# Kernel tuning notes

Hardware: AMD Instinct MI355X
Metric: run time of the kernel (lower is better)

The kernel has to match this reference:

```python
import jax, jax.numpy as jnp
import numpy as np

N, D, K, NUM_CB = 65536, 256, 1024, 3

def setup_inputs() -> dict:
    key = jax.random.key(0)
    k1, k2 = jax.random.split(key)
    z = jax.random.normal(k1, (N, D), dtype=jnp.float32)
    # torch init: uniform_(-1/codebook_size, 1/codebook_size)
    codebooks = jax.random.uniform(k2, (NUM_CB, K, D), dtype=jnp.float32,
                                   minval=-1.0 / K, maxval=1.0 / K)
    return {"z": z, "codebooks": codebooks}

def reference(z, codebooks):
    """Residual VQ quantize() of RVQ_VAE: 3 sequential codebook stages with
    straight-through estimator. Returns (final_quantized, codebook_loss, commitment_loss)."""
    sg = jax.lax.stop_gradient
    final_quantized = jnp.zeros_like(z)
    codebook_losses = jnp.asarray(0.0, z.dtype)
    commitment_losses = jnp.asarray(0.0, z.dtype)
    for i in range(codebooks.shape[0]):  # small fixed number of residual stages
        cb = codebooks[i]                               # [K, D]
        # squared L2 distances via the matmul expansion (as in the torch code)
        l2 = jnp.sum(z * z, axis=1, keepdims=True)      # [N, 1]
        c2 = jnp.sum(cb * cb, axis=1)[None, :]          # [1, K]
        cl = z @ cb.T                                   # [N, K] GEMM
        distances = l2 - 2.0 * cl + c2                  # [N, K]
        closest = jnp.argmin(distances, axis=-1)        # [N]
        # one-hot @ codebook in the original == direct gather (same math)
        codes = cb[closest]                             # [N, D]
        codebook_losses = codebook_losses + jnp.mean((codes - sg(z)) ** 2)
        commitment_losses = commitment_losses + jnp.mean((sg(codes) - z) ** 2)
        codes_st = z + sg(codes - z)                    # straight-through
        final_quantized = final_quantized + codes_st
        z = z - sg(codes_st)                            # residual for next stage
    return final_quantized, codebook_losses, commitment_losses
```

## Files before the change

### kernel.cpp

```cpp
#include <hip/hip_runtime.h>
#include <stdint.h>

#define DDIM 256
#define KCODES 1024
#define OUTOFF 16777216
#define ZT 131072

typedef __attribute__((ext_vector_type(8))) _Float16 f16x8;
typedef __attribute__((ext_vector_type(4))) float f32x4;

__device__ inline void gld16(const void* g, void* l) {
  __builtin_amdgcn_global_load_lds(
      (const __attribute__((address_space(1))) unsigned int*)g,
      (__attribute__((address_space(3))) unsigned int*)l, 16, 0, 0);
}

__global__ __launch_bounds__(256) void k_prep(const float* __restrict__ cbs,
                                              unsigned short* __restrict__ ch,
                                              float* __restrict__ c2h,
                                              float* __restrict__ out) {
  if (blockIdx.x == 0 && threadIdx.x == 0) { out[OUTOFF] = 0.f; out[OUTOFF + 1] = 0.f; }
  int code = blockIdx.x * 4 + (threadIdx.x >> 6);
  int lane = threadIdx.x & 63;
  float4 v = ((const float4*)(cbs + (size_t)code * DDIM))[lane];
  ushort4 u;
  u.x = __builtin_bit_cast(unsigned short, (_Float16)(v.x * -1024.0f));
  u.y = __builtin_bit_cast(unsigned short, (_Float16)(v.y * -1024.0f));
  u.z = __builtin_bit_cast(unsigned short, (_Float16)(v.z * -1024.0f));
  u.w = __builtin_bit_cast(unsigned short, (_Float16)(v.w * -1024.0f));
  int r = code & 15;
  int g = lane >> 1;
  size_t byteoff = (size_t)(code >> 4) * 8192 + (size_t)r * 512 +
                   (size_t)((g ^ ((r & 7) << 2)) << 4) + (size_t)(lane & 1) * 8;
  *(ushort4*)((char*)ch + byteoff) = u;
  double s = (double)v.x * v.x + (double)v.y * v.y + (double)v.z * v.z + (double)v.w * v.w;
  for (int off = 1; off < 64; off <<= 1) s += __shfl_xor(s, off);
  if (lane == 0) c2h[code] = (float)(s * 512.0);
}

__global__ __launch_bounds__(512, 2) void k_rvq(const float* __restrict__ z0,
                                                const float* __restrict__ cbs,
                                                const unsigned short* __restrict__ ch,
                                                const float* __restrict__ c2h,
                                                float* __restrict__ outq) {
  __shared__ char lds[163840];
  float* s_wv8 = (float*)(lds + 122880);
  int* s_wk8 = (int*)(lds + 124928);
  int* s_bk = (int*)(lds + 126976);
  float* s_ls = (float*)(lds + 127232);

  const int tid = threadIdx.x;
  const int w = tid >> 6;
  const int lane = tid & 63;
  const int l15 = lane & 15;
  const int lg = lane >> 4;
  const int erow = w * 8 + (lane & 7);
  const int ecb = lane >> 3;
  const size_t gbase = (size_t)blockIdx.x * 64 * DDIM;
  const size_t elane = gbase + (size_t)erow * DDIM + ecb * 32;
  char* myslab = lds + w * 16384;

  float4 f[8];
#pragma unroll
  for (int q = 0; q < 8; ++q) f[q] = *(const float4*)(z0 + elane + q * 4);

  float lsum = 0.f;

  for (int s = 0; s < 3; ++s) {
#pragma unroll
    for (int g2 = 0; g2 < 4; ++g2) {
      float4 va = f[2 * g2], vb = f[2 * g2 + 1];
      f16x8 hv;
      hv[0] = (_Float16)va.x; hv[1] = (_Float16)va.y; hv[2] = (_Float16)va.z; hv[3] = (_Float16)va.w;
      hv[4] = (_Float16)vb.x; hv[5] = (_Float16)vb.y; hv[6] = (_Float16)vb.z; hv[7] = (_Float16)vb.w;
      int g = ecb * 4 + g2;
      *(f16x8*)(lds + ZT + erow * 512 + ((g ^ ((erow & 7) << 2)) << 4)) = hv;
    }
    __syncthreads();

    f16x8 b[4][8];
#pragma unroll
    for (int i = 0; i < 4; ++i)
#pragma unroll
      for (int kc = 0; kc < 8; ++kc) {
        int row = i * 16 + l15;
        int g = kc * 4 + lg;
        b[i][kc] = *(const f16x8*)(lds + ZT + row * 512 + ((g ^ ((row & 7) << 2)) << 4));
      }

    const char* chS = (const char*)ch + (size_t)s * 524288;
    const float* c2S = c2h + s * KCODES;
    float bv[4];
    int bk[4];
#pragma unroll
    for (int i = 0; i < 4; ++i) { bv[i] = 3.4e38f; bk[i] = 0x3FFFFFFF; }

    float4 c2cur = *(const float4*)(c2S + w * 128 + lg * 4);
    {
      const char* src = chS + (size_t)w * 8 * 8192;
#pragma unroll
      for (int i = 0; i < 8; ++i)
        gld16(src + lane * 16 + i * 1024, myslab + lane * 16 + i * 1024);
    }

    for (int c = 0; c < 8; ++c) {
      float4 c2next;
      if (c < 7) {
        c2next = *(const float4*)(c2S + w * 128 + (c + 1) * 16 + lg * 4);
        const char* src = chS + (size_t)(w * 8 + c + 1) * 8192;
        char* dst = myslab + ((c + 1) & 1) * 8192;
#pragma unroll
        for (int i = 0; i < 8; ++i)
          gld16(src + lane * 16 + i * 1024, dst + lane * 16 + i * 1024);
        asm volatile("s_waitcnt vmcnt(9)" ::: "memory");
      } else {
        asm volatile("s_waitcnt vmcnt(0)" ::: "memory");
      }
      __builtin_amdgcn_sched_barrier(0);

      f32x4 acc[4];
      f32x4 cv = {c2cur.x, c2cur.y, c2cur.z, c2cur.w};
#pragma unroll
      for (int i = 0; i < 4; ++i) acc[i] = cv;
      const char* slab = myslab + (c & 1) * 8192;
#pragma unroll
      for (int kc = 0; kc < 8; ++kc) {
        f16x8 a = *(const f16x8*)(slab + l15 * 512 + (((kc * 4 + lg) ^ ((l15 & 7) << 2)) << 4));
#pragma unroll
        for (int i = 0; i < 4; ++i)
          acc[i] = __builtin_amdgcn_mfma_f32_16x16x32_f16(a, b[i][kc], acc[i], 0, 0, 0);
      }
#pragma unroll
      for (int r = 0; r < 4; ++r) {
        int kcode = w * 128 + c * 16 + lg * 4 + r;
#pragma unroll
        for (int i = 0; i < 4; ++i) {
          float v = acc[i][r];
          if (v < bv[i]) { bv[i] = v; bk[i] = kcode; }
        }
      }
      if (c < 7) c2cur = c2next;
    }
    __syncthreads();

#pragma unroll
    for (int m = 16; m <= 32; m <<= 1)
#pragma unroll
      for (int i = 0; i < 4; ++i) {
        float ov = __shfl_xor(bv[i], m);
        int ok = __shfl_xor(bk[i], m);
        if (ov < bv[i] || (ov == bv[i] && ok < bk[i])) { bv[i] = ov; bk[i] = ok; }
      }
    if (lane < 16)
#pragma unroll
      for (int i = 0; i < 4; ++i) {
        s_wv8[w * 64 + i * 16 + lane] = bv[i];
        s_wk8[w * 64 + i * 16 + lane] = bk[i];
      }
    __syncthreads();
    if (tid < 64) {
      float v = s_wv8[tid];
      int k = s_wk8[tid];
#pragma unroll
      for (int w2 = 1; w2 < 8; ++w2) {
        float vv = s_wv8[w2 * 64 + tid];
        int kk = s_wk8[w2 * 64 + tid];
        if (vv < v || (vv == v && kk < k)) { v = vv; k = kk; }
      }
      s_bk[tid] = k;
    }
    __syncthreads();

    float lacc = 0.f;
    {
      const float* cbsS = cbs + (size_t)s * (KCODES * DDIM);
      int code = s_bk[erow];
      const float* cp = cbsS + (size_t)code * DDIM + ecb * 32;
#pragma unroll
      for (int q = 0; q < 8; ++q) {
        float4 cv2 = *(const float4*)(cp + q * 4);
        float4 zv = f[q];
        float tx = cv2.x - zv.x, ty = cv2.y - zv.y, tz = cv2.z - zv.z, tw = cv2.w - zv.w;
        lacc += (tx * tx + ty * ty) + (tz * tz + tw * tw);
        float cstx = zv.x + tx, csty = zv.y + ty, cstz = zv.z + tz, cstw = zv.w + tw;
        float znx = zv.x - cstx, zny = zv.y - csty, znz = zv.z - cstz, znw = zv.w - cstw;
        if (s < 2) {
          f[q].x = znx; f[q].y = zny; f[q].z = znz; f[q].w = znw;
        } else {
          float4 a = *(const float4*)(z0 + elane + q * 4);
          float4 o;
          o.x = a.x - znx; o.y = a.y - zny; o.z = a.z - znz; o.w = a.w - znw;
          *(float4*)(outq + elane + q * 4) = o;
        }
      }
    }
#pragma unroll
    for (int m = 1; m < 64; m <<= 1) lacc += __shfl_xor(lacc, m);
    if (lane == 0) s_ls[w] = lacc;
    __syncthreads();
    if (tid == 0)
      lsum += ((s_ls[0] + s_ls[1]) + (s_ls[2] + s_ls[3])) +
              ((s_ls[4] + s_ls[5]) + (s_ls[6] + s_ls[7]));
  }

  if (tid == 0) {
    float v = lsum * (1.0f / 16777216.0f);
    atomicAdd(outq + OUTOFF, v);
    atomicAdd(outq + OUTOFF + 1, v);
  }
}

extern "C" void kernel_launch(void* const* d_in, const int* in_sizes, int n_in,
                              void* d_out, int out_size, void* d_ws, size_t ws_size,
                              hipStream_t stream) {
  const float* z0 = (const float*)d_in[0];
  const float* cbs = (const float*)d_in[1];
  float* out = (float*)d_out;
  char* ws = (char*)d_ws;
  unsigned short* ch = (unsigned short*)ws;
  float* c2h = (float*)(ws + 1572864);

  k_prep<<<768, 256, 0, stream>>>(cbs, ch, c2h, out);
  k_rvq<<<1024, 512, 0, stream>>>(z0, cbs, ch, c2h, out);
}
```

Measured before the change: 382.8 us.

## Store residual as fp16 hi in LDS plus fp16 lo in registers, simplify swizzle

The fp32 residual (32 floats per lane) is replaced by an fp16 high part kept in the LDS tile used for MFMA and an fp16 low part held in registers, cutting register pressure and removing the per-stage repack. The LDS swizzle changes from XOR with (r&7)<<2 to XOR with r&7, and the per-stage loss reduction through LDS plus a barrier is deferred to the end of the kernel. Launch bounds switch to the amdgpu_waves_per_eu attribute. The hi+lo split drops a little precision versus fp32 residuals, which could flip argmin near-ties.

```diff
diff --git a/kernel.cpp b/kernel.cpp
--- a/kernel.cpp
+++ b/kernel.cpp
@@ -4,7 +4,7 @@
 #define DDIM 256
 #define KCODES 1024
 #define OUTOFF 16777216
-#define ZT 131072
+#define HT 131072
 
 typedef __attribute__((ext_vector_type(8))) _Float16 f16x8;
 typedef __attribute__((ext_vector_type(4))) float f32x4;
@@ -31,18 +31,20 @@
   int r = code & 15;
   int g = lane >> 1;
   size_t byteoff = (size_t)(code >> 4) * 8192 + (size_t)r * 512 +
-                   (size_t)((g ^ ((r & 7) << 2)) << 4) + (size_t)(lane & 1) * 8;
+                   (size_t)((g ^ (r & 7)) << 4) + (size_t)(lane & 1) * 8;
   *(ushort4*)((char*)ch + byteoff) = u;
   double s = (double)v.x * v.x + (double)v.y * v.y + (double)v.z * v.z + (double)v.w * v.w;
   for (int off = 1; off < 64; off <<= 1) s += __shfl_xor(s, off);
   if (lane == 0) c2h[code] = (float)(s * 512.0);
 }
 
-__global__ __launch_bounds__(512, 2) void k_rvq(const float* __restrict__ z0,
-                                                const float* __restrict__ cbs,
-                                                const unsigned short* __restrict__ ch,
-                                                const float* __restrict__ c2h,
-                                                float* __restrict__ outq) {
+__global__ __launch_bounds__(512)
+__attribute__((amdgpu_waves_per_eu(2, 2)))
+void k_rvq(const float* __restrict__ z0,
+           const float* __restrict__ cbs,
+           const unsigned short* __restrict__ ch,
+           const float* __restrict__ c2h,
+           float* __restrict__ outq) {
   __shared__ char lds[163840];
   float* s_wv8 = (float*)(lds + 122880);
   int* s_wk8 = (int*)(lds + 124928);
@@ -57,36 +59,38 @@
   const int erow = w * 8 + (lane & 7);
   const int ecb = lane >> 3;
   const size_t gbase = (size_t)blockIdx.x * 64 * DDIM;
-  const size_t elane = gbase + (size_t)erow * DDIM + ecb * 32;
+  const size_t ebase = gbase + (size_t)erow * DDIM + ecb * 32;
   char* myslab = lds + w * 16384;
-
-  float4 f[8];
-#pragma unroll
-  for (int q = 0; q < 8; ++q) f[q] = *(const float4*)(z0 + elane + q * 4);
-
-  float lsum = 0.f;
+  char* hirow = lds + HT + erow * 512;
+
+  f16x8 lo[4];
+#pragma unroll
+  for (int q = 0; q < 4; ++q) {
+    float4 va = *(const float4*)(z0 + ebase + q * 8);
+    float4 vb = *(const float4*)(z0 + ebase + q * 8 + 4);
+    f16x8 hv, lv;
+    hv[0] = (_Float16)va.x; hv[1] = (_Float16)va.y; hv[2] = (_Float16)va.z; hv[3] = (_Float16)va.w;
+    hv[4] = (_Float16)vb.x; hv[5] = (_Float16)vb.y; hv[6] = (_Float16)vb.z; hv[7] = (_Float16)vb.w;
+    lv[0] = (_Float16)(va.x - (float)hv[0]); lv[1] = (_Float16)(va.y - (float)hv[1]);
+    lv[2] = (_Float16)(va.z - (float)hv[2]); lv[3] = (_Float16)(va.w - (float)hv[3]);
+    lv[4] = (_Float16)(vb.x - (float)hv[4]); lv[5] = (_Float16)(vb.y - (float)hv[5]);
+    lv[6] = (_Float16)(vb.z - (float)hv[6]); lv[7] = (_Float16)(vb.w - (float)hv[7]);
+    *(f16x8*)(hirow + (((ecb * 4 + q) ^ (erow & 7)) << 4)) = hv;
+    lo[q] = lv;
+  }
+
+  float wloss = 0.f;
 
   for (int s = 0; s < 3; ++s) {
-#pragma unroll
-    for (int g2 = 0; g2 < 4; ++g2) {
-      float4 va = f[2 * g2], vb = f[2 * g2 + 1];
-      f16x8 hv;
-      hv[0] = (_Float16)va.x; hv[1] = (_Float16)va.y; hv[2] = (_Float16)va.z; hv[3] = (_Float16)va.w;
-      hv[4] = (_Float16)vb.x; hv[5] = (_Float16)vb.y; hv[6] = (_Float16)vb.z; hv[7] = (_Float16)vb.w;
-      int g = ecb * 4 + g2;
-      *(f16x8*)(lds + ZT + erow * 512 + ((g ^ ((erow & 7) << 2)) << 4)) = hv;
-    }
     __syncthreads();
 
     f16x8 b[4][8];
 #pragma unroll
     for (int i = 0; i < 4; ++i)
 #pragma unroll
-      for (int kc = 0; kc < 8; ++kc) {
-        int row = i * 16 + l15;
-        int g = kc * 4 + lg;
-        b[i][kc] = *(const f16x8*)(lds + ZT + row * 512 + ((g ^ ((row & 7) << 2)) << 4));
-      }
+      for (int kc = 0; kc < 8; ++kc)
+        b[i][kc] = *(const f16x8*)(lds + HT + (i * 16 + l15) * 512 +
+                                   (((kc * 4 + lg) ^ (l15 & 7)) << 4));
 
     const char* chS = (const char*)ch + (size_t)s * 524288;
     const float* c2S = c2h + s * KCODES;
@@ -125,7 +129,7 @@
       const char* slab = myslab + (c & 1) * 8192;
 #pragma unroll
       for (int kc = 0; kc < 8; ++kc) {
-        f16x8 a = *(const f16x8*)(slab + l15 * 512 + (((kc * 4 + lg) ^ ((l15 & 7) << 2)) << 4));
+        f16x8 a = *(const f16x8*)(slab + l15 * 512 + (((kc * 4 + lg) ^ (l15 & 7)) << 4));
 #pragma unroll
         for (int i = 0; i < 4; ++i)
           acc[i] = __builtin_amdgcn_mfma_f32_16x16x32_f16(a, b[i][kc], acc[i], 0, 0, 0);
@@ -173,38 +177,57 @@
 
     float lacc = 0.f;
     {
-      const float* cbsS = cbs + (size_t)s * (KCODES * DDIM);
       int code = s_bk[erow];
-      const float* cp = cbsS + (size_t)code * DDIM + ecb * 32;
-#pragma unroll
-      for (int q = 0; q < 8; ++q) {
-        float4 cv2 = *(const float4*)(cp + q * 4);
-        float4 zv = f[q];
-        float tx = cv2.x - zv.x, ty = cv2.y - zv.y, tz = cv2.z - zv.z, tw = cv2.w - zv.w;
-        lacc += (tx * tx + ty * ty) + (tz * tz + tw * tw);
-        float cstx = zv.x + tx, csty = zv.y + ty, cstz = zv.z + tz, cstw = zv.w + tw;
-        float znx = zv.x - cstx, zny = zv.y - csty, znz = zv.z - cstz, znw = zv.w - cstw;
+      const float* cp = cbs + (size_t)s * (KCODES * DDIM) + (size_t)code * DDIM + ecb * 32;
+#pragma unroll
+      for (int q = 0; q < 4; ++q) {
+        int slot = ((ecb * 4 + q) ^ (erow & 7)) << 4;
+        f16x8 hv = *(const f16x8*)(hirow + slot);
+        float zz[8], cc[8], zn[8];
+#pragma unroll
+        for (int k2 = 0; k2 < 8; ++k2) zz[k2] = (float)hv[k2] + (float)lo[q][k2];
+        float4 c0 = *(const float4*)(cp + q * 8);
+        float4 c1 = *(const float4*)(cp + q * 8 + 4);
+        cc[0] = c0.x; cc[1] = c0.y; cc[2] = c0.z; cc[3] = c0.w;
+        cc[4] = c1.x; cc[5] = c1.y; cc[6] = c1.z; cc[7] = c1.w;
+#pragma unroll
+        for (int k2 = 0; k2 < 8; ++k2) {
+          float t = cc[k2] - zz[k2];
+          lacc += t * t;
+          float cst = zz[k2] + t;
+          zn[k2] = zz[k2] - cst;
+        }
         if (s < 2) {
-          f[q].x = znx; f[q].y = zny; f[q].z = znz; f[q].w = znw;
+          f16x8 nh, nl;
+#pragma unroll
+          for (int k2 = 0; k2 < 8; ++k2) {
+            nh[k2] = (_Float16)zn[k2];
+            nl[k2] = (_Float16)(zn[k2] - (float)nh[k2]);
+          }
+          *(f16x8*)(hirow + slot) = nh;
+          lo[q] = nl;
         } else {
-          float4 a = *(const float4*)(z0 + elane + q * 4);
-          float4 o;
-          o.x = a.x - znx; o.y = a.y - zny; o.z = a.z - znz; o.w = a.w - znw;
-          *(float4*)(outq + elane + q * 4) = o;
+          float4 a0 = *(const float4*)(z0 + ebase + q * 8);
+          float4 a1 = *(const float4*)(z0 + ebase + q * 8 + 4);
+          float4 o0, o1;
+          o0.x = a0.x - zn[0]; o0.y = a0.y - zn[1]; o0.z = a0.z - zn[2]; o0.w = a0.w - zn[3];
+          o1.x = a1.x - zn[4]; o1.y = a1.y - zn[5]; o1.z = a1.z - zn[6]; o1.w = a1.w - zn[7];
+          *(float4*)(outq + ebase + q * 8) = o0;
+          *(float4*)(outq + ebase + q * 8 + 4) = o1;
         }
       }
     }
 #pragma unroll
     for (int m = 1; m < 64; m <<= 1) lacc += __shfl_xor(lacc, m);
-    if (lane == 0) s_ls[w] = lacc;
-    __syncthreads();
-    if (tid == 0)
-      lsum += ((s_ls[0] + s_ls[1]) + (s_ls[2] + s_ls[3])) +
+    wloss += lacc;
+  }
+
+  if (lane == 0) s_ls[w] = wloss;
+  __syncthreads();
+  if (tid == 0) {
+    float t = ((s_ls[0] + s_ls[1]) + (s_ls[2] + s_ls[3])) +
               ((s_ls[4] + s_ls[5]) + (s_ls[6] + s_ls[7]));
-  }
-
-  if (tid == 0) {
-    float v = lsum * (1.0f / 16777216.0f);
+    float v = t * (1.0f / 16777216.0f);
     atomicAdd(outq + OUTOFF, v);
     atomicAdd(outq + OUTOFF + 1, v);
   }
```

Result: faster. 366.6 us (-4.2%).
